# Performance work log

Measured on AMD Instinct MI355X. Metric: run time of the kernel, lower is better.

Reference implementation:

```python
import jax, jax.numpy as jnp
import numpy as np

B, N, D, H = 2048, 64, 256, 16

def setup_inputs() -> dict:
    key = jax.random.key(0)
    ks = jax.random.split(key, 6)
    members_embeds = jax.random.normal(ks[0], (B, N, D), dtype=jnp.float32)
    item_embeds = jax.random.normal(ks[1], (B, D), dtype=jnp.float32)
    # MLP params: Linear(D,16) -> ReLU -> Linear(16,1)
    W1 = jax.random.normal(ks[2], (D, H), dtype=jnp.float32) * (1.0 / np.sqrt(D))
    b1 = jnp.zeros((H,), dtype=jnp.float32)
    W2 = jax.random.normal(ks[3], (H, 1), dtype=jnp.float32) * (1.0 / np.sqrt(H))
    b2 = jnp.zeros((1,), dtype=jnp.float32)
    return {"members_embeds": members_embeds, "item_embeds": item_embeds,
            "W1": W1, "b1": b1, "W2": W2, "b2": b2}

def reference(members_embeds, item_embeds, W1, b1, W2, b2):
    # Original: diff_i = sum_{j != i} (u_i - u_j) * item  ==  (N*u_i - sum_j u_j) * item
    n = members_embeds.shape[1]
    total = jnp.sum(members_embeds, axis=1, keepdims=True)           # [B,1,D]
    diff = (n * members_embeds - total) * item_embeds[:, None, :]    # [B,N,D]
    h = jax.nn.relu(jnp.einsum('bnd,dh->bnh', diff, W1) + b1)        # [B,N,16]
    logits = (jnp.einsum('bnh,ho->bno', h, W2) + b2)[..., 0]         # [B,N]
    return jax.nn.softmax(logits, axis=1)                            # weights over members
```

## Files before the change

kernel.cpp:

```cpp
#include <hip/hip_runtime.h>


static constexpr int NMEM  = 64;
static constexpr int DDIM  = 256;
static constexpr int TD    = 32;
static constexpr int NTILE = DDIM / TD;
static constexpr int UTS   = 36;
static constexpr int UTS4  = UTS / 4;

__device__ __forceinline__ void fma4(float4& acc, float s, const float4& w) {
    acc.x = fmaf(s, w.x, acc.x);
    acc.y = fmaf(s, w.y, acc.y);
    acc.z = fmaf(s, w.z, acc.z);
    acc.w = fmaf(s, w.w, acc.w);
}

__global__ __launch_bounds__(256, 2)
void attn_group_softmax(const float* __restrict__ u_g,
                        const float* __restrict__ item_g,
                        const float* __restrict__ W1,
                        const float* __restrict__ b1,
                        const float* __restrict__ W2,
                        float* __restrict__ out)
{
    __shared__ float w1s[DDIM * 16];
    __shared__ float item_s[4][DDIM];
    __shared__ float ut[4][NMEM * UTS];

    const int tid  = threadIdx.x;
    const int w    = tid >> 6;
    const int lane = tid & 63;
    const int b    = blockIdx.x * 4 + w;

    {
        const float4* src = (const float4*)W1;
        float4* dst = (float4*)w1s;
        #pragma unroll
        for (int i = 0; i < 4; ++i) dst[tid + 256 * i] = src[tid + 256 * i];
    }
    {
        const float4* src = (const float4*)(item_g + (size_t)b * DDIM);
        ((float4*)item_s[w])[lane] = src[lane];
    }
    __syncthreads();

    const int q    = lane & 3;
    const int n0   = lane >> 2;
    const int col4 = lane & 7;
    const int row0 = lane >> 3;

    const float4* ug4  = (const float4*)u_g + (size_t)b * (NMEM * DDIM / 4);
    const float4* it4p = (const float4*)item_s[w];
    float4*       uts4 = (float4*)ut[w];
    const float4* utf4 = (const float4*)ut[w];
    const float4* w1s4 = (const float4*)w1s;

    float4 acc0 = make_float4(0.f, 0.f, 0.f, 0.f);
    float4 acc1 = acc0, acc2 = acc0, acc3 = acc0;

    float4 r[8];
    #pragma unroll
    for (int i = 0; i < 8; ++i)
        r[i] = ug4[(row0 + 8 * i) * (DDIM / 4) + col4];

    for (int t = 0; t < NTILE; ++t) {
        const float4 itv = it4p[t * 8 + col4];
        #pragma unroll
        for (int i = 0; i < 8; ++i) {
            float4 v = r[i];
            v.x *= itv.x; v.y *= itv.y; v.z *= itv.z; v.w *= itv.w;
            uts4[(row0 + 8 * i) * UTS4 + col4] = v;
        }
        __syncthreads();

        if (t + 1 < NTILE) {
            #pragma unroll
            for (int i = 0; i < 8; ++i)
                r[i] = ug4[(row0 + 8 * i) * (DDIM / 4) + (t + 1) * 8 + col4];
        }

        #pragma unroll
        for (int d4 = 0; d4 < TD / 4; ++d4) {
            const float4 ua = utf4[(n0     ) * UTS4 + d4];
            const float4 ub = utf4[(n0 + 16) * UTS4 + d4];
            const float4 uc = utf4[(n0 + 32) * UTS4 + d4];
            const float4 ud = utf4[(n0 + 48) * UTS4 + d4];
            const int dbase = (t * TD + d4 * 4) * 4 + q;
            const float4 w0  = w1s4[dbase];
            const float4 w1r = w1s4[dbase + 4];
            const float4 w2r = w1s4[dbase + 8];
            const float4 w3r = w1s4[dbase + 12];
            fma4(acc0, ua.x, w0); fma4(acc0, ua.y, w1r); fma4(acc0, ua.z, w2r); fma4(acc0, ua.w, w3r);
            fma4(acc1, ub.x, w0); fma4(acc1, ub.y, w1r); fma4(acc1, ub.z, w2r); fma4(acc1, ub.w, w3r);
            fma4(acc2, uc.x, w0); fma4(acc2, uc.y, w1r); fma4(acc2, uc.z, w2r); fma4(acc2, uc.w, w3r);
            fma4(acc3, ud.x, w0); fma4(acc3, ud.y, w1r); fma4(acc3, ud.z, w2r); fma4(acc3, ud.w, w3r);
        }
        __syncthreads();
    }

    float4 tt;
    tt.x = acc0.x + acc1.x + acc2.x + acc3.x;
    tt.y = acc0.y + acc1.y + acc2.y + acc3.y;
    tt.z = acc0.z + acc1.z + acc2.z + acc3.z;
    tt.w = acc0.w + acc1.w + acc2.w + acc3.w;
    #pragma unroll
    for (int off = 4; off <= 32; off <<= 1) {
        tt.x += __shfl_xor(tt.x, off, 64);
        tt.y += __shfl_xor(tt.y, off, 64);
        tt.z += __shfl_xor(tt.z, off, 64);
        tt.w += __shfl_xor(tt.w, off, 64);
    }

    const float4 b1v = ((const float4*)b1)[q];
    const float4 w2v = ((const float4*)W2)[q];

    auto logit_part = [&](const float4& a) -> float {
        const float zx = fmaxf(fmaf(64.f, a.x, b1v.x - tt.x), 0.f);
        const float zy = fmaxf(fmaf(64.f, a.y, b1v.y - tt.y), 0.f);
        const float zz = fmaxf(fmaf(64.f, a.z, b1v.z - tt.z), 0.f);
        const float zw = fmaxf(fmaf(64.f, a.w, b1v.w - tt.w), 0.f);
        return zx * w2v.x + zy * w2v.y + zz * w2v.z + zw * w2v.w;
    };

    float p0 = logit_part(acc0);
    float p1 = logit_part(acc1);
    float p2 = logit_part(acc2);
    float p3 = logit_part(acc3);
    p0 += __shfl_xor(p0, 1, 64); p0 += __shfl_xor(p0, 2, 64);
    p1 += __shfl_xor(p1, 1, 64); p1 += __shfl_xor(p1, 2, 64);
    p2 += __shfl_xor(p2, 1, 64); p2 += __shfl_xor(p2, 2, 64);
    p3 += __shfl_xor(p3, 1, 64); p3 += __shfl_xor(p3, 2, 64);

    float m = fmaxf(fmaxf(p0, p1), fmaxf(p2, p3));
    #pragma unroll
    for (int off = 4; off <= 32; off <<= 1) m = fmaxf(m, __shfl_xor(m, off, 64));
    const float e0 = __expf(p0 - m);
    const float e1 = __expf(p1 - m);
    const float e2 = __expf(p2 - m);
    const float e3 = __expf(p3 - m);
    float s = e0 + e1 + e2 + e3;
    #pragma unroll
    for (int off = 4; off <= 32; off <<= 1) s += __shfl_xor(s, off, 64);
    const float inv = 1.0f / s;

    if (q == 0) {
        float* ob = out + (size_t)b * NMEM + n0;
        ob[0]  = e0 * inv;
        ob[16] = e1 * inv;
        ob[32] = e2 * inv;
        ob[48] = e3 * inv;
    }
}

extern "C" void kernel_launch(void* const* d_in, const int* in_sizes, int n_in,
                              void* d_out, int out_size, void* d_ws, size_t ws_size,
                              hipStream_t stream) {
    const float* u    = (const float*)d_in[0];
    const float* item = (const float*)d_in[1];
    const float* W1   = (const float*)d_in[2];
    const float* b1   = (const float*)d_in[3];
    const float* W2   = (const float*)d_in[4];
    (void)in_sizes; (void)n_in; (void)out_size; (void)d_ws; (void)ws_size;

    attn_group_softmax<<<512, 256, 0, stream>>>(u, item, W1, b1, W2, (float*)d_out);
}
```

Before: 203.8 us.

## Split D across lane quads and keep full 16-wide accumulators in registers

Replaces the shared-memory staging of item-scaled member tiles with direct per-thread global loads, where each lane quad splits the D dimension and every thread accumulates all 16 hidden outputs for 4 members in registers. The partial sums are then combined with cross-lane shuffles. This removes the per-tile __syncthreads and the LDS round trip for the u tile, and pads W1 rows in shared memory to limit bank conflicts. In exchange it uses 64 accumulator registers plus a prefetch buffer, which may cut occupancy below the 2-blocks launch bound. Global loads become 16-byte strided per lane, which is less coalesced, and the end of the kernel needs many more shuffles.

```diff
diff --git a/kernel.cpp b/kernel.cpp
--- a/kernel.cpp
+++ b/kernel.cpp
@@ -1,19 +1,10 @@
 #include <hip/hip_runtime.h>
 
 
-static constexpr int NMEM  = 64;
-static constexpr int DDIM  = 256;
-static constexpr int TD    = 32;
-static constexpr int NTILE = DDIM / TD;
-static constexpr int UTS   = 36;
-static constexpr int UTS4  = UTS / 4;
-
-__device__ __forceinline__ void fma4(float4& acc, float s, const float4& w) {
-    acc.x = fmaf(s, w.x, acc.x);
-    acc.y = fmaf(s, w.y, acc.y);
-    acc.z = fmaf(s, w.z, acc.z);
-    acc.w = fmaf(s, w.w, acc.w);
-}
+static constexpr int NMEM = 64;
+static constexpr int DDIM = 256;
+static constexpr int HD   = 16;
+static constexpr int W1S  = 20;
 
 __global__ __launch_bounds__(256, 2)
 void attn_group_softmax(const float* __restrict__ u_g,
@@ -23,9 +14,7 @@
                         const float* __restrict__ W2,
                         float* __restrict__ out)
 {
-    __shared__ float w1s[DDIM * 16];
-    __shared__ float item_s[4][DDIM];
-    __shared__ float ut[4][NMEM * UTS];
+    __shared__ __align__(16) float w1s[DDIM * W1S];
 
     const int tid  = threadIdx.x;
     const int w    = tid >> 6;
@@ -33,115 +22,129 @@
     const int b    = blockIdx.x * 4 + w;
 
     {
-        const float4* src = (const float4*)W1;
-        float4* dst = (float4*)w1s;
+        const float4* src = (const float4*)(W1 + tid * HD);
+        float4*       dst = (float4*)(w1s + tid * W1S);
         #pragma unroll
-        for (int i = 0; i < 4; ++i) dst[tid + 256 * i] = src[tid + 256 * i];
-    }
-    {
-        const float4* src = (const float4*)(item_g + (size_t)b * DDIM);
-        ((float4*)item_s[w])[lane] = src[lane];
+        for (int c = 0; c < 4; ++c) dst[c] = src[c];
     }
     __syncthreads();
 
-    const int q    = lane & 3;
-    const int n0   = lane >> 2;
-    const int col4 = lane & 7;
-    const int row0 = lane >> 3;
+    const int q  = lane & 3;
+    const int n0 = lane >> 2;
 
-    const float4* ug4  = (const float4*)u_g + (size_t)b * (NMEM * DDIM / 4);
-    const float4* it4p = (const float4*)item_s[w];
-    float4*       uts4 = (float4*)ut[w];
-    const float4* utf4 = (const float4*)ut[w];
-    const float4* w1s4 = (const float4*)w1s;
+    const float4* ug4 = (const float4*)u_g + (size_t)b * (NMEM * DDIM / 4);
+    const float4* it4 = (const float4*)item_g + (size_t)b * (DDIM / 4);
 
-    float4 acc0 = make_float4(0.f, 0.f, 0.f, 0.f);
-    float4 acc1 = acc0, acc2 = acc0, acc3 = acc0;
+    float acc[4][16];
+    #pragma unroll
+    for (int k = 0; k < 4; ++k)
+        #pragma unroll
+        for (int h = 0; h < 16; ++h) acc[k][h] = 0.f;
 
-    float4 r[8];
+    float4 ub[4][4];
+    float4 itb[4];
     #pragma unroll
-    for (int i = 0; i < 8; ++i)
-        r[i] = ug4[(row0 + 8 * i) * (DDIM / 4) + col4];
+    for (int jj = 0; jj < 2; ++jj) {
+        #pragma unroll
+        for (int k = 0; k < 4; ++k)
+            ub[jj][k] = ug4[(n0 + 16 * k) * 64 + jj * 4 + q];
+        itb[jj] = it4[jj * 4 + q];
+    }
 
-    for (int t = 0; t < NTILE; ++t) {
-        const float4 itv = it4p[t * 8 + col4];
+    #pragma unroll 4
+    for (int j = 0; j < 16; ++j) {
+        const int cur = j & 3;
+        const int nxt = (j + 2) & 3;
+        if (j + 2 < 16) {
+            #pragma unroll
+            for (int k = 0; k < 4; ++k)
+                ub[nxt][k] = ug4[(n0 + 16 * k) * 64 + (j + 2) * 4 + q];
+            itb[nxt] = it4[(j + 2) * 4 + q];
+        }
+
+        const float4 itv = itb[cur];
+        float s[4][4];
         #pragma unroll
-        for (int i = 0; i < 8; ++i) {
-            float4 v = r[i];
-            v.x *= itv.x; v.y *= itv.y; v.z *= itv.z; v.w *= itv.w;
-            uts4[(row0 + 8 * i) * UTS4 + col4] = v;
-        }
-        __syncthreads();
-
-        if (t + 1 < NTILE) {
-            #pragma unroll
-            for (int i = 0; i < 8; ++i)
-                r[i] = ug4[(row0 + 8 * i) * (DDIM / 4) + (t + 1) * 8 + col4];
+        for (int k = 0; k < 4; ++k) {
+            s[k][0] = ub[cur][k].x * itv.x;
+            s[k][1] = ub[cur][k].y * itv.y;
+            s[k][2] = ub[cur][k].z * itv.z;
+            s[k][3] = ub[cur][k].w * itv.w;
         }
 
         #pragma unroll
-        for (int d4 = 0; d4 < TD / 4; ++d4) {
-            const float4 ua = utf4[(n0     ) * UTS4 + d4];
-            const float4 ub = utf4[(n0 + 16) * UTS4 + d4];
-            const float4 uc = utf4[(n0 + 32) * UTS4 + d4];
-            const float4 ud = utf4[(n0 + 48) * UTS4 + d4];
-            const int dbase = (t * TD + d4 * 4) * 4 + q;
-            const float4 w0  = w1s4[dbase];
-            const float4 w1r = w1s4[dbase + 4];
-            const float4 w2r = w1s4[dbase + 8];
-            const float4 w3r = w1s4[dbase + 12];
-            fma4(acc0, ua.x, w0); fma4(acc0, ua.y, w1r); fma4(acc0, ua.z, w2r); fma4(acc0, ua.w, w3r);
-            fma4(acc1, ub.x, w0); fma4(acc1, ub.y, w1r); fma4(acc1, ub.z, w2r); fma4(acc1, ub.w, w3r);
-            fma4(acc2, uc.x, w0); fma4(acc2, uc.y, w1r); fma4(acc2, uc.z, w2r); fma4(acc2, uc.w, w3r);
-            fma4(acc3, ud.x, w0); fma4(acc3, ud.y, w1r); fma4(acc3, ud.z, w2r); fma4(acc3, ud.w, w3r);
+        for (int e = 0; e < 4; ++e) {
+            const int d = 16 * j + 4 * q + e;
+            const float4* wrow = (const float4*)(w1s + d * W1S);
+            #pragma unroll
+            for (int hc = 0; hc < 4; ++hc) {
+                const float4 wv = wrow[hc];
+                #pragma unroll
+                for (int k = 0; k < 4; ++k) {
+                    acc[k][4 * hc + 0] = fmaf(s[k][e], wv.x, acc[k][4 * hc + 0]);
+                    acc[k][4 * hc + 1] = fmaf(s[k][e], wv.y, acc[k][4 * hc + 1]);
+                    acc[k][4 * hc + 2] = fmaf(s[k][e], wv.z, acc[k][4 * hc + 2]);
+                    acc[k][4 * hc + 3] = fmaf(s[k][e], wv.w, acc[k][4 * hc + 3]);
+                }
+            }
         }
-        __syncthreads();
     }
 
-    float4 tt;
-    tt.x = acc0.x + acc1.x + acc2.x + acc3.x;
-    tt.y = acc0.y + acc1.y + acc2.y + acc3.y;
-    tt.z = acc0.z + acc1.z + acc2.z + acc3.z;
-    tt.w = acc0.w + acc1.w + acc2.w + acc3.w;
     #pragma unroll
-    for (int off = 4; off <= 32; off <<= 1) {
-        tt.x += __shfl_xor(tt.x, off, 64);
-        tt.y += __shfl_xor(tt.y, off, 64);
-        tt.z += __shfl_xor(tt.z, off, 64);
-        tt.w += __shfl_xor(tt.w, off, 64);
+    for (int k = 0; k < 4; ++k)
+        #pragma unroll
+        for (int h = 0; h < 16; ++h) {
+            float v = acc[k][h];
+            v += __shfl_xor(v, 1, 64);
+            v += __shfl_xor(v, 2, 64);
+            acc[k][h] = v;
+        }
+
+    float tt[16];
+    #pragma unroll
+    for (int h = 0; h < 16; ++h) {
+        float v = acc[0][h] + acc[1][h] + acc[2][h] + acc[3][h];
+        #pragma unroll
+        for (int off = 4; off <= 32; off <<= 1) v += __shfl_xor(v, off, 64);
+        tt[h] = v;
     }
 
-    const float4 b1v = ((const float4*)b1)[q];
-    const float4 w2v = ((const float4*)W2)[q];
+    float b1c[16], w2c[16];
+    {
+        const float4* b4 = (const float4*)b1;
+        const float4* w4 = (const float4*)W2;
+        #pragma unroll
+        for (int c = 0; c < 4; ++c) {
+            const float4 t1 = b4[c], t2 = w4[c];
+            b1c[4*c+0] = t1.x; b1c[4*c+1] = t1.y; b1c[4*c+2] = t1.z; b1c[4*c+3] = t1.w;
+            w2c[4*c+0] = t2.x; w2c[4*c+1] = t2.y; w2c[4*c+2] = t2.z; w2c[4*c+3] = t2.w;
+        }
+    }
 
-    auto logit_part = [&](const float4& a) -> float {
-        const float zx = fmaxf(fmaf(64.f, a.x, b1v.x - tt.x), 0.f);
-        const float zy = fmaxf(fmaf(64.f, a.y, b1v.y - tt.y), 0.f);
-        const float zz = fmaxf(fmaf(64.f, a.z, b1v.z - tt.z), 0.f);
-        const float zw = fmaxf(fmaf(64.f, a.w, b1v.w - tt.w), 0.f);
-        return zx * w2v.x + zy * w2v.y + zz * w2v.z + zw * w2v.w;
-    };
+    float p[4];
+    #pragma unroll
+    for (int k = 0; k < 4; ++k) {
+        float sum = 0.f;
+        #pragma unroll
+        for (int h = 0; h < 16; ++h) {
+            float z = fmaf(64.f, acc[k][h], b1c[h] - tt[h]);
+            z = fmaxf(z, 0.f);
+            sum = fmaf(z, w2c[h], sum);
+        }
+        p[k] = sum;
+    }
 
-    float p0 = logit_part(acc0);
-    float p1 = logit_part(acc1);
-    float p2 = logit_part(acc2);
-    float p3 = logit_part(acc3);
-    p0 += __shfl_xor(p0, 1, 64); p0 += __shfl_xor(p0, 2, 64);
-    p1 += __shfl_xor(p1, 1, 64); p1 += __shfl_xor(p1, 2, 64);
-    p2 += __shfl_xor(p2, 1, 64); p2 += __shfl_xor(p2, 2, 64);
-    p3 += __shfl_xor(p3, 1, 64); p3 += __shfl_xor(p3, 2, 64);
-
-    float m = fmaxf(fmaxf(p0, p1), fmaxf(p2, p3));
+    float m = fmaxf(fmaxf(p[0], p[1]), fmaxf(p[2], p[3]));
     #pragma unroll
     for (int off = 4; off <= 32; off <<= 1) m = fmaxf(m, __shfl_xor(m, off, 64));
-    const float e0 = __expf(p0 - m);
-    const float e1 = __expf(p1 - m);
-    const float e2 = __expf(p2 - m);
-    const float e3 = __expf(p3 - m);
-    float s = e0 + e1 + e2 + e3;
+    const float e0 = __expf(p[0] - m);
+    const float e1 = __expf(p[1] - m);
+    const float e2 = __expf(p[2] - m);
+    const float e3 = __expf(p[3] - m);
+    float sden = e0 + e1 + e2 + e3;
     #pragma unroll
-    for (int off = 4; off <= 32; off <<= 1) s += __shfl_xor(s, off, 64);
-    const float inv = 1.0f / s;
+    for (int off = 4; off <= 32; off <<= 1) sden += __shfl_xor(sden, off, 64);
+    const float inv = 1.0f / sden;
 
     if (q == 0) {
         float* ob = out + (size_t)b * NMEM + n0;
```

Measured after the change: 311.9 us. 53.0% more time.
